# Kernel optimization log

Measured on AMD Instinct MI355X. Metric: run time of the kernel, lower is better.

## Reference

```python
import jax, jax.numpy as jnp
import numpy as np


def conv1x1(x, w, b):
    # x: (B, C_in, D, H, W), w: (C_out, C_in), b: (C_out,)  -- 1x1x1 Conv3d == per-voxel linear
    return jnp.einsum('bcdhw,oc->bodhw', x, w) + b[None, :, None, None, None]


def setup_inputs() -> dict:
    key = jax.random.key(0)
    ks = jax.random.split(key, 6)
    B, C, D, H, W = 2, 64, 8, 64, 64
    K = 4096  # codebook_size after halving
    return {
        'z': jax.random.normal(ks[0], (B, C, D, H, W), dtype=jnp.float32),
        'embedding': jax.random.normal(ks[1], (K, C), dtype=jnp.float32),
        'pre_w': jax.random.normal(ks[2], (C, C), dtype=jnp.float32) * (1.0 / np.sqrt(C)),
        'pre_b': jax.random.normal(ks[3], (C,), dtype=jnp.float32) * 0.01,
        'post_w': jax.random.normal(ks[4], (C, C), dtype=jnp.float32) * (1.0 / np.sqrt(C)),
        'post_b': jax.random.normal(ks[5], (C,), dtype=jnp.float32) * 0.01,
    }


def reference(z, embedding, pre_w, pre_b, post_w, post_b):
    B, C, D, H, W = z.shape
    x = conv1x1(z, pre_w, pre_b)  # pre_quant_conv

    # ---- quantize() ----
    # tokens: (B*D*H*W, C)
    t = jnp.transpose(x, (0, 2, 3, 4, 1)).reshape(-1, C)
    # squared euclidean distances (argmin identical to torch.cdist argmin)
    dist2 = (jnp.sum(t * t, axis=-1, keepdims=True)
             - 2.0 * t @ embedding.T
             + jnp.sum(embedding * embedding, axis=-1)[None, :])  # (N, K)
    idx = jnp.argmin(dist2, axis=-1)  # (N,)
    q = embedding[idx]  # gather: (N, C)

    commitment_loss = jnp.mean((jax.lax.stop_gradient(q) - t) ** 2)
    codebook_loss = jnp.mean((q - jax.lax.stop_gradient(t)) ** 2)

    # straight-through estimator
    q = t + jax.lax.stop_gradient(q - t)
    quant = jnp.transpose(q.reshape(B, D, H, W, C), (0, 4, 1, 2, 3))

    out = conv1x1(quant, post_w, post_b)  # post_quant_conv
    indices = idx.reshape(B, D, H, W)
    return out, codebook_loss, commitment_loss, indices
```

## Files before the change

kernel.cpp:

```cpp
#include <hip/hip_runtime.h>
#include <cstdint>
#include <cstddef>

typedef float  f32x4  __attribute__((ext_vector_type(4)));
typedef float  f32x16 __attribute__((ext_vector_type(16)));
typedef short  s16x8  __attribute__((ext_vector_type(8)));

#define DEV __device__ __forceinline__

static constexpr int    DHW       = 32768;
static constexpr int    NTOK      = 65536;
static constexpr int    CHUNK_B   = 18432;
static constexpr size_t OUT_ELEMS = 4194304;
static constexpr float  BIGC      = 512.0f;
static constexpr float  TAU       = 0.015f;
static constexpr int    FLAG_CAP  = 7424;

static constexpr size_t WS_PREP = 0;
static constexpr size_t WS_RESW = 1179648;
static constexpr size_t WS_RESB = 2228224;
static constexpr size_t WS_PART = 2490368;
static constexpr size_t WS_CNT  = 2494464;
static constexpr size_t WS_FLAG = 2494720;

DEV unsigned f2bf(float f) {
  unsigned u = __float_as_uint(f);
  return (u + 0x7FFFu + ((u >> 16) & 1u)) >> 16;
}
DEV float bf2f(unsigned h) { return __uint_as_float(h << 16); }
DEV unsigned med3u(unsigned a, unsigned b, unsigned c) {
  unsigned r;
  asm("v_med3_u32 %0, %1, %2, %3" : "=v"(r) : "v"(a), "v"(b), "v"(c));
  return r;
}
DEV void gl_lds16(const void* g, void* l) {
  __builtin_amdgcn_global_load_lds(
      (const __attribute__((address_space(1))) unsigned int*)g,
      (__attribute__((address_space(3))) unsigned int*)l, 16, 0, 0);
}

__global__ __launch_bounds__(256) void k_pre(const float* __restrict__ z,
    const float* __restrict__ emb, const float* __restrict__ pw, const float* __restrict__ pb,
    float* __restrict__ dout, char* __restrict__ ws)
{
  const int blk = blockIdx.x, tid = threadIdx.x;
  if (blk == 0 && tid == 0) *(int*)(ws + WS_CNT) = 0;
  if (blk < 256) {
    float* t = dout;
    const int v = blk * 256 + tid;
    const int b = v >> 15, r = v & (DHW - 1);
    const float* zp = z + (size_t)b * 64 * DHW + r;
    float zr[64];
#pragma unroll
    for (int c2 = 0; c2 < 64; ++c2) zr[c2] = zp[(size_t)c2 * DHW];
    for (int c = 0; c < 64; c += 4) {
      const float* w0 = pw + c * 64;
      const float* w1 = pw + (c + 1) * 64;
      const float* w2 = pw + (c + 2) * 64;
      const float* w3 = pw + (c + 3) * 64;
      float a0 = pb[c], a1 = pb[c + 1], a2 = pb[c + 2], a3 = pb[c + 3];
#pragma unroll
      for (int c2 = 0; c2 < 64; ++c2) {
        const float zv = zr[c2];
        a0 = fmaf(w0[c2], zv, a0); a1 = fmaf(w1[c2], zv, a1);
        a2 = fmaf(w2[c2], zv, a2); a3 = fmaf(w3[c2], zv, a3);
      }
      t[(size_t)c * NTOK + v]       = a0;
      t[(size_t)(c + 1) * NTOK + v] = a1;
      t[(size_t)(c + 2) * NTOK + v] = a2;
      t[(size_t)(c + 3) * NTOK + v] = a3;
    }
  } else {
    const int tt = (blk - 256) * 256 + tid;
#pragma unroll
    for (int uu = 0; uu < 2; ++uu) {
      const int u = tt * 2 + uu;
      const int k = u >> 3, j = u & 7;
      const float* ep = emb + (size_t)k * 64 + j * 8;
      unsigned hw[4], lw[4];
#pragma unroll
      for (int i = 0; i < 4; ++i) {
        float g0 = -2.0f * ep[2 * i], g1 = -2.0f * ep[2 * i + 1];
        unsigned h0 = f2bf(g0); unsigned l0 = f2bf(g0 - bf2f(h0));
        unsigned h1 = f2bf(g1); unsigned l1 = f2bf(g1 - bf2f(h1));
        hw[i] = h0 | (h1 << 16); lw[i] = l0 | (l1 << 16);
      }
      char* base = ws + WS_PREP + (size_t)(k >> 6) * CHUNK_B;
      const int r = k & 63;
      const int swz = (r & 15) << 4;
      char* rowp = base + r * 256;
      *(uint4*)(rowp + ((j * 16) ^ swz))        = make_uint4(hw[0], hw[1], hw[2], hw[3]);
      *(uint4*)(rowp + ((128 + j * 16) ^ swz))  = make_uint4(lw[0], lw[1], lw[2], lw[3]);
      if (j == 0) {
        const float* er = emb + (size_t)k * 64;
        float s = 0.f;
#pragma unroll
        for (int c = 0; c < 64; ++c) s = fmaf(er[c], er[c], s);
        s += BIGC;
        unsigned eh  = f2bf(s);
        float    rs  = s - bf2f(eh);
        unsigned el  = f2bf(rs);
        unsigned el2 = f2bf(rs - bf2f(el));
        *(uint4*)(base + 16384 + r * 16) = make_uint4(eh | (el << 16), el2, 0u, 0u);
        if (r == 0) *(uint4*)(base + 16384 + 1024) = make_uint4(0u, 0u, 0u, 0u);
      }
    }
  }
}

__global__ __launch_bounds__(512, 4) void k_dist(float* __restrict__ dout,
                                                 char* __restrict__ ws)
{
  constexpr int NCH = 32;
  __shared__ __align__(16) char smem[2 * CHUNK_B];
  const float* t = dout;
  const int tid = threadIdx.x;
  const int w = tid >> 6, lane = tid & 63;
  const int l31 = lane & 31, khalf = lane >> 5;
  const int gidx = blockIdx.x >> 1, h = blockIdx.x & 1;
  const int tb = gidx * 256 + w * 32;
  const int tok = tb + l31;

  s16x8 tav[4], tlv[4];
#pragma unroll
  for (int kt = 0; kt < 4; ++kt) {
    const float* tc = t + (size_t)(kt * 16 + khalf * 8) * NTOK + tok;
    float f[8];
#pragma unroll
    for (int i = 0; i < 8; ++i) f[i] = tc[(size_t)i * NTOK];
    union { unsigned u[4]; s16x8 v; } xh, xl;
#pragma unroll
    for (int i = 0; i < 4; ++i) {
      unsigned h0 = f2bf(f[2 * i]),     l0 = f2bf(f[2 * i]     - bf2f(h0));
      unsigned h1 = f2bf(f[2 * i + 1]), l1 = f2bf(f[2 * i + 1] - bf2f(h1));
      xh.u[i] = h0 | (h1 << 16); xl.u[i] = l0 | (l1 << 16);
    }
    tav[kt] = xh.v; tlv[kt] = xl.v;
  }
  s16x8 ones;
  { union { unsigned u[4]; s16x8 v; } o;
    o.u[0] = khalf ? 0u : 0x3F803F80u;
    o.u[1] = khalf ? 0u : 0x00003F80u;
    o.u[2] = 0u; o.u[3] = 0u; ones = o.v; }

  const char* prep = ws + WS_PREP + (size_t)h * NCH * CHUNK_B;
  const int swz = (l31 & 15) << 4;

  {
    const char* src = prep;
    gl_lds16(src + w * 1024 + lane * 16, smem + w * 1024);
    gl_lds16(src + 8192 + w * 1024 + lane * 16, smem + 8192 + w * 1024);
    if (w < 2) gl_lds16(src + 16384 + w * 1024 + lane * 16, smem + 16384 + w * 1024);
  }
  __syncthreads();

  unsigned u1 = 0x7f800000u, u2 = 0x7f800000u;
  int c1 = 0;

  for (int c = 0; c < NCH; ++c) {
    const char* L = smem + (c & 1) * CHUNK_B;
    if (c + 1 < NCH) {
      const char* src = prep + (size_t)(c + 1) * CHUNK_B;
      char* dst = smem + ((c + 1) & 1) * CHUNK_B;
      gl_lds16(src + w * 1024 + lane * 16, dst + w * 1024);
      gl_lds16(src + 8192 + w * 1024 + lane * 16, dst + 8192 + w * 1024);
      if (w < 2) gl_lds16(src + 16384 + w * 1024 + lane * 16, dst + 16384 + w * 1024);
    }
    f32x16 acc0 = {}, acc1 = {};
    {
      const s16x8 e0 = *(const s16x8*)(L + (khalf ? (16384 + 1024) : (16384 + l31 * 16)));
      const s16x8 e1 = *(const s16x8*)(L + (khalf ? (16384 + 1024) : (16384 + (32 + l31) * 16)));
      acc0 = __builtin_amdgcn_mfma_f32_32x32x16_bf16(e0, ones, acc0, 0, 0, 0);
      acc1 = __builtin_amdgcn_mfma_f32_32x32x16_bf16(e1, ones, acc1, 0, 0, 0);
    }
#pragma unroll
    for (int kt = 0; kt < 4; ++kt) {
      const int i0 = (kt * 32 + khalf * 16) ^ swz;
      const s16x8 gh0 = *(const s16x8*)(L + l31 * 256 + i0);
      const s16x8 gl0 = *(const s16x8*)(L + l31 * 256 + (i0 ^ 128));
      const s16x8 gh1 = *(const s16x8*)(L + (32 + l31) * 256 + i0);
      const s16x8 gl1 = *(const s16x8*)(L + (32 + l31) * 256 + (i0 ^ 128));
      acc0 = __builtin_amdgcn_mfma_f32_32x32x16_bf16(gh0, tav[kt], acc0, 0, 0, 0);
      acc0 = __builtin_amdgcn_mfma_f32_32x32x16_bf16(gh0, tlv[kt], acc0, 0, 0, 0);
      acc0 = __builtin_amdgcn_mfma_f32_32x32x16_bf16(gl0, tav[kt], acc0, 0, 0, 0);
      acc1 = __builtin_amdgcn_mfma_f32_32x32x16_bf16(gh1, tav[kt], acc1, 0, 0, 0);
      acc1 = __builtin_amdgcn_mfma_f32_32x32x16_bf16(gh1, tlv[kt], acc1, 0, 0, 0);
      acc1 = __builtin_amdgcn_mfma_f32_32x32x16_bf16(gl1, tav[kt], acc1, 0, 0, 0);
    }
    const unsigned p1 = u1;
#pragma unroll
    for (int q = 0; q < 16; ++q) {
      const unsigned w0 = (unsigned)((q & 3) + 8 * (q >> 2));
      unsigned v0 = (__float_as_uint(acc0[q]) & ~63u) | w0;
      u2 = med3u(u1, v0, u2); u1 = u1 < v0 ? u1 : v0;
      unsigned v1 = (__float_as_uint(acc1[q]) & ~63u) | (w0 + 32u);
      u2 = med3u(u1, v1, u2); u1 = u1 < v1 ? u1 : v1;
    }
    if (u1 != p1) c1 = c;
    __syncthreads();
  }

  u1 |= (unsigned)(khalf * 4);
  const unsigned o1 = __shfl_xor(u1, 32);
  const unsigned o2 = __shfl_xor(u2, 32);
  const int      oc = __shfl_xor(c1, 32);
  const unsigned am = u1 & ~63u, om = o1 & ~63u;
  const int mycode = c1 * 64 + (int)(u1 & 63u);
  const int ocode  = oc * 64 + (int)(o1 & 63u);
  const bool owins = (om < am) || (om == am && ocode < mycode);
  const unsigned f1 = owins ? o1 : u1;
  const int      fc = owins ? oc : c1;
  const unsigned mx = owins ? am : om;
  unsigned s2 = (u2 & ~63u) < (o2 & ~63u) ? (u2 & ~63u) : (o2 & ~63u);
  s2 = s2 < mx ? s2 : mx;
  if (khalf == 0) {
    const bool nt = (__uint_as_float(s2) - __uint_as_float(f1 & ~63u)) < TAU;
    ((unsigned*)(ws + WS_RESW))[h * 65536 + tok] = f1;
    ((unsigned char*)(ws + WS_RESB))[h * 65536 + tok] =
        (unsigned char)(fc | (nt ? 0x80 : 0));
  }
}

__global__ __launch_bounds__(256) void k_merge(const float* __restrict__ emb,
    float* __restrict__ dout, char* __restrict__ ws)
{
  __shared__ float ls[4];
  const int tid = threadIdx.x;
  const int v = blockIdx.x * 64 + (tid >> 2);
  const int q4 = tid & 3;
  const unsigned* resw = (const unsigned*)(ws + WS_RESW);
  const unsigned char* resb = (const unsigned char*)(ws + WS_RESB);
  const unsigned A = resw[v], B = resw[65536 + v];
  const unsigned am = A & ~63u, bm = B & ~63u;
  const bool bwins = bm < am;
  const unsigned bw = bwins ? B : A;
  const int bq = bwins ? 1 : 0;
  const unsigned k1 = bwins ? bm : am;
  const unsigned k2 = bwins ? am : bm;
  const unsigned char bb = resb[bq * 65536 + v];
  const int code = bq * 2048 + (int)(bb & 31u) * 64 + (int)(bw & 63u);
  const float* tcol = dout + v;
  const float* qe = emb + (size_t)code * 64 + q4 * 16;
  float acc = 0.f;
#pragma unroll
  for (int i = 0; i < 4; ++i) {
    const float4 qv = *(const float4*)(qe + i * 4);
#pragma unroll
    for (int j = 0; j < 4; ++j) {
      const int ch = q4 * 16 + i * 4 + j;
      const float d = tcol[(size_t)ch * NTOK] - ((const float*)&qv)[j];
      acc = fmaf(d, d, acc);
    }
  }
  acc += __shfl_xor(acc, 1);
  acc += __shfl_xor(acc, 2);
  if (q4 == 0) {
    dout[OUT_ELEMS + 2 + v] = (float)code;
    const bool flag = (bb & 0x80u) ||
                      (__uint_as_float(k2) - __uint_as_float(k1) < TAU);
    if (flag) {
      int p = atomicAdd((int*)(ws + WS_CNT), 1);
      if (p < FLAG_CAP) ((int*)(ws + WS_FLAG))[p] = v;
    }
  }
#pragma unroll
  for (int m = 4; m < 64; m <<= 1) acc += __shfl_xor(acc, m);
  const int lane = tid & 63, wv = tid >> 6;
  if (lane == 0) ls[wv] = acc;
  __syncthreads();
  if (tid == 0)
    ((float*)(ws + WS_PART))[blockIdx.x] = (ls[0] + ls[1] + ls[2] + ls[3]) * 0.25f;
}

__global__ __launch_bounds__(256) void k_refine(const float* __restrict__ z,
    const float* __restrict__ emb, const float* __restrict__ pw, const float* __restrict__ pb,
    float* __restrict__ dout, char* __restrict__ ws)
{
  __shared__ double tdsh[64];
  __shared__ double dred[4]; __shared__ int kred[4];
  int cv = *(const int*)(ws + WS_CNT);
  if (cv > FLAG_CAP) cv = FLAG_CAP;
  const int slot = blockIdx.x;
  if (slot >= cv) return;
  const int tid = threadIdx.x;
  const int lane = tid & 63, wv = tid >> 6;
  const int n = ((const int*)(ws + WS_FLAG))[slot];

  if (tid < 64) {
    const int b = n >> 15, r = n & (DHW - 1);
    const float* zp = z + (size_t)b * 64 * DHW + r;
    const float* wr = pw + tid * 64;
    double a = (double)pb[tid];
    for (int c2 = 0; c2 < 64; ++c2)
      a = fma((double)wr[c2], (double)zp[(size_t)c2 * DHW], a);
    tdsh[tid] = a;
  }
  __syncthreads();

  double td[64];
#pragma unroll
  for (int j = 0; j < 64; ++j) td[j] = tdsh[j];

  double dmin = 1e300; int kmin = 0;
  for (int it = 0; it < 16; ++it) {
    const int code = it * 256 + tid;
    const float4* e = (const float4*)(emb + (size_t)code * 64);
    double d0 = 0.0, d1 = 0.0;
#pragma unroll
    for (int i = 0; i < 16; ++i) {
      const float4 ev = e[i];
      const double x0 = td[4 * i]     - (double)ev.x; d0 = fma(x0, x0, d0);
      const double x1 = td[4 * i + 1] - (double)ev.y; d1 = fma(x1, x1, d1);
      const double x2 = td[4 * i + 2] - (double)ev.z; d0 = fma(x2, x2, d0);
      const double x3 = td[4 * i + 3] - (double)ev.w; d1 = fma(x3, x3, d1);
    }
    const double d = d0 + d1;
    if (d < dmin) { dmin = d; kmin = code; }
  }
#pragma unroll
  for (int m = 1; m < 64; m <<= 1) {
    const double od = __shfl_xor(dmin, m);
    const int    ok = __shfl_xor(kmin, m);
    if (od < dmin || (od == dmin && ok < kmin)) { dmin = od; kmin = ok; }
  }
  if (lane == 0) { dred[wv] = dmin; kred[wv] = kmin; }
  __syncthreads();
  if (tid == 0) {
#pragma unroll
    for (int i = 1; i < 4; ++i)
      if (dred[i] < dmin || (dred[i] == dmin && kred[i] < kmin)) { dmin = dred[i]; kmin = kred[i]; }
    dout[OUT_ELEMS + 2 + n] = (float)kmin;
  }
}

__global__ __launch_bounds__(256) void k_post(const float* __restrict__ emb,
    const float* __restrict__ ow, const float* __restrict__ ob,
    float* __restrict__ dout, const char* __restrict__ ws)
{
  __shared__ float ps[256];
  const int v = blockIdx.x * 256 + threadIdx.x;
  const int b = v >> 15, r = v & (DHW - 1);
  const int code = (int)dout[OUT_ELEMS + 2 + v];
  const float* q = emb + (size_t)code * 64;
  float qr[64];
#pragma unroll
  for (int i = 0; i < 16; ++i) *(float4*)(qr + i * 4) = *(const float4*)(q + i * 4);
  float* op = dout + (size_t)b * 64 * DHW + r;
  for (int o = 0; o < 64; o += 4) {
    const float* w0 = ow + o * 64;
    const float* w1 = ow + (o + 1) * 64;
    const float* w2 = ow + (o + 2) * 64;
    const float* w3 = ow + (o + 3) * 64;
    float a0 = ob[o], a1 = ob[o + 1], a2 = ob[o + 2], a3 = ob[o + 3];
#pragma unroll
    for (int cch = 0; cch < 64; ++cch) {
      const float qv = qr[cch];
      a0 = fmaf(w0[cch], qv, a0); a1 = fmaf(w1[cch], qv, a1);
      a2 = fmaf(w2[cch], qv, a2); a3 = fmaf(w3[cch], qv, a3);
    }
    op[(size_t)o * DHW]       = a0;
    op[(size_t)(o + 1) * DHW] = a1;
    op[(size_t)(o + 2) * DHW] = a2;
    op[(size_t)(o + 3) * DHW] = a3;
  }
  if (blockIdx.x == 0) {
    const float* part = (const float*)(ws + WS_PART);
    const int t4 = threadIdx.x * 4;
    float s = ((part[t4] + part[t4 + 1]) + part[t4 + 2]) + part[t4 + 3];
    ps[threadIdx.x] = s;
    __syncthreads();
    if (threadIdx.x == 0) {
      float tot = 0.f;
      for (int i = 0; i < 256; ++i) tot += ps[i];
      const float mean = tot / 4194304.0f;
      dout[OUT_ELEMS]     = mean;
      dout[OUT_ELEMS + 1] = mean;
    }
  }
}

extern "C" void kernel_launch(void* const* d_in, const int* in_sizes, int n_in,
                              void* d_out, int out_size, void* d_ws, size_t ws_size,
                              hipStream_t stream) {
  (void)in_sizes; (void)n_in; (void)out_size; (void)ws_size;
  const float* z   = (const float*)d_in[0];
  const float* emb = (const float*)d_in[1];
  const float* pw  = (const float*)d_in[2];
  const float* pb  = (const float*)d_in[3];
  const float* ow  = (const float*)d_in[4];
  const float* ob  = (const float*)d_in[5];
  float* out = (float*)d_out;
  char*  ws  = (char*)d_ws;

  hipLaunchKernelGGL(k_pre,    dim3(320),  dim3(256), 0, stream, z, emb, pw, pb, out, ws);
  hipLaunchKernelGGL(k_dist,   dim3(512),  dim3(512), 0, stream, out, ws);
  hipLaunchKernelGGL(k_merge,  dim3(1024), dim3(256), 0, stream, emb, out, ws);
  hipLaunchKernelGGL(k_refine, dim3(FLAG_CAP), dim3(256), 0, stream, z, emb, pw, pb, out, ws);
  hipLaunchKernelGGL(k_post,   dim3(256),  dim3(256), 0, stream, emb, ow, ob, out, ws);
}
```

Before: 196.6 us.

## Split codebook rows across wave pairs so each wave covers two token fragments

The distance kernel's work split changes. Each pair of waves now shares 64 tokens, and each wave handles 32 codebook rows per chunk against two 32-token fragments, where before each wave covered all 64 rows for 32 tokens. Every LDS codebook fragment load now feeds twice as many MFMAs, halving LDS read traffic per MFMA. In exchange, each wave holds twice the token operands in registers and needs an extra cross-wave argmin merge through shared memory with a block barrier. The merge kernel's partial-loss scaling also changes by dropping the 0.25 factor, which alters the loss output unless it is compensated in code not shown.

```diff
diff --git a/kernel.cpp b/kernel.cpp
--- a/kernel.cpp
+++ b/kernel.cpp
@@ -113,29 +113,33 @@
 {
   constexpr int NCH = 32;
   __shared__ __align__(16) char smem[2 * CHUNK_B];
+  __shared__ unsigned xch[4][64][3];
   const float* t = dout;
   const int tid = threadIdx.x;
   const int w = tid >> 6, lane = tid & 63;
   const int l31 = lane & 31, khalf = lane >> 5;
+  const int pair = w >> 1, p = w & 1;
   const int gidx = blockIdx.x >> 1, h = blockIdx.x & 1;
-  const int tb = gidx * 256 + w * 32;
-  const int tok = tb + l31;
-
-  s16x8 tav[4], tlv[4];
-#pragma unroll
-  for (int kt = 0; kt < 4; ++kt) {
-    const float* tc = t + (size_t)(kt * 16 + khalf * 8) * NTOK + tok;
-    float f[8];
-#pragma unroll
-    for (int i = 0; i < 8; ++i) f[i] = tc[(size_t)i * NTOK];
-    union { unsigned u[4]; s16x8 v; } xh, xl;
-#pragma unroll
-    for (int i = 0; i < 4; ++i) {
-      unsigned h0 = f2bf(f[2 * i]),     l0 = f2bf(f[2 * i]     - bf2f(h0));
-      unsigned h1 = f2bf(f[2 * i + 1]), l1 = f2bf(f[2 * i + 1] - bf2f(h1));
-      xh.u[i] = h0 | (h1 << 16); xl.u[i] = l0 | (l1 << 16);
-    }
-    tav[kt] = xh.v; tlv[kt] = xl.v;
+  const int tb = gidx * 256 + pair * 64;
+
+  s16x8 tav[2][4], tlv[2][4];
+#pragma unroll
+  for (int tf = 0; tf < 2; ++tf) {
+#pragma unroll
+    for (int kt = 0; kt < 4; ++kt) {
+      const float* tc = t + (size_t)(kt * 16 + khalf * 8) * NTOK + (tb + tf * 32 + l31);
+      float f[8];
+#pragma unroll
+      for (int i = 0; i < 8; ++i) f[i] = tc[(size_t)i * NTOK];
+      union { unsigned u[4]; s16x8 v; } xh, xl;
+#pragma unroll
+      for (int i = 0; i < 4; ++i) {
+        unsigned h0 = f2bf(f[2 * i]),     l0 = f2bf(f[2 * i]     - bf2f(h0));
+        unsigned h1 = f2bf(f[2 * i + 1]), l1 = f2bf(f[2 * i + 1] - bf2f(h1));
+        xh.u[i] = h0 | (h1 << 16); xl.u[i] = l0 | (l1 << 16);
+      }
+      tav[tf][kt] = xh.v; tlv[tf][kt] = xl.v;
+    }
   }
   s16x8 ones;
   { union { unsigned u[4]; s16x8 v; } o;
@@ -144,7 +148,9 @@
     o.u[2] = 0u; o.u[3] = 0u; ones = o.v; }
 
   const char* prep = ws + WS_PREP + (size_t)h * NCH * CHUNK_B;
-  const int swz = (l31 & 15) << 4;
+  const int swz  = (l31 & 15) << 4;
+  const int rowb = (p * 32 + l31) * 256;
+  const int eoff = khalf ? (16384 + 1024) : (16384 + (p * 32 + l31) * 16);
 
   {
     const char* src = prep;
@@ -154,8 +160,9 @@
   }
   __syncthreads();
 
-  unsigned u1 = 0x7f800000u, u2 = 0x7f800000u;
-  int c1 = 0;
+  unsigned u1[2] = {0x7f800000u, 0x7f800000u};
+  unsigned u2[2] = {0x7f800000u, 0x7f800000u};
+  int c1[2] = {0, 0};
 
   for (int c = 0; c < NCH; ++c) {
     const char* L = smem + (c & 1) * CHUNK_B;
@@ -168,56 +175,86 @@
     }
     f32x16 acc0 = {}, acc1 = {};
     {
-      const s16x8 e0 = *(const s16x8*)(L + (khalf ? (16384 + 1024) : (16384 + l31 * 16)));
-      const s16x8 e1 = *(const s16x8*)(L + (khalf ? (16384 + 1024) : (16384 + (32 + l31) * 16)));
+      const s16x8 e0 = *(const s16x8*)(L + eoff);
       acc0 = __builtin_amdgcn_mfma_f32_32x32x16_bf16(e0, ones, acc0, 0, 0, 0);
-      acc1 = __builtin_amdgcn_mfma_f32_32x32x16_bf16(e1, ones, acc1, 0, 0, 0);
+      acc1 = __builtin_amdgcn_mfma_f32_32x32x16_bf16(e0, ones, acc1, 0, 0, 0);
     }
 #pragma unroll
     for (int kt = 0; kt < 4; ++kt) {
       const int i0 = (kt * 32 + khalf * 16) ^ swz;
-      const s16x8 gh0 = *(const s16x8*)(L + l31 * 256 + i0);
-      const s16x8 gl0 = *(const s16x8*)(L + l31 * 256 + (i0 ^ 128));
-      const s16x8 gh1 = *(const s16x8*)(L + (32 + l31) * 256 + i0);
-      const s16x8 gl1 = *(const s16x8*)(L + (32 + l31) * 256 + (i0 ^ 128));
-      acc0 = __builtin_amdgcn_mfma_f32_32x32x16_bf16(gh0, tav[kt], acc0, 0, 0, 0);
-      acc0 = __builtin_amdgcn_mfma_f32_32x32x16_bf16(gh0, tlv[kt], acc0, 0, 0, 0);
-      acc0 = __builtin_amdgcn_mfma_f32_32x32x16_bf16(gl0, tav[kt], acc0, 0, 0, 0);
-      acc1 = __builtin_amdgcn_mfma_f32_32x32x16_bf16(gh1, tav[kt], acc1, 0, 0, 0);
-      acc1 = __builtin_amdgcn_mfma_f32_32x32x16_bf16(gh1, tlv[kt], acc1, 0, 0, 0);
-      acc1 = __builtin_amdgcn_mfma_f32_32x32x16_bf16(gl1, tav[kt], acc1, 0, 0, 0);
-    }
-    const unsigned p1 = u1;
+      const s16x8 gh = *(const s16x8*)(L + rowb + i0);
+      const s16x8 gl = *(const s16x8*)(L + rowb + (i0 ^ 128));
+      acc0 = __builtin_amdgcn_mfma_f32_32x32x16_bf16(gh, tav[0][kt], acc0, 0, 0, 0);
+      acc0 = __builtin_amdgcn_mfma_f32_32x32x16_bf16(gh, tlv[0][kt], acc0, 0, 0, 0);
+      acc0 = __builtin_amdgcn_mfma_f32_32x32x16_bf16(gl, tav[0][kt], acc0, 0, 0, 0);
+      acc1 = __builtin_amdgcn_mfma_f32_32x32x16_bf16(gh, tav[1][kt], acc1, 0, 0, 0);
+      acc1 = __builtin_amdgcn_mfma_f32_32x32x16_bf16(gh, tlv[1][kt], acc1, 0, 0, 0);
+      acc1 = __builtin_amdgcn_mfma_f32_32x32x16_bf16(gl, tav[1][kt], acc1, 0, 0, 0);
+    }
+    const unsigned pa = u1[0], pb2 = u1[1];
 #pragma unroll
     for (int q = 0; q < 16; ++q) {
       const unsigned w0 = (unsigned)((q & 3) + 8 * (q >> 2));
       unsigned v0 = (__float_as_uint(acc0[q]) & ~63u) | w0;
-      u2 = med3u(u1, v0, u2); u1 = u1 < v0 ? u1 : v0;
-      unsigned v1 = (__float_as_uint(acc1[q]) & ~63u) | (w0 + 32u);
-      u2 = med3u(u1, v1, u2); u1 = u1 < v1 ? u1 : v1;
-    }
-    if (u1 != p1) c1 = c;
+      u2[0] = med3u(u1[0], v0, u2[0]); u1[0] = u1[0] < v0 ? u1[0] : v0;
+      unsigned v1 = (__float_as_uint(acc1[q]) & ~63u) | w0;
+      u2[1] = med3u(u1[1], v1, u2[1]); u1[1] = u1[1] < v1 ? u1[1] : v1;
+    }
+    if (u1[0] != pa)  c1[0] = c;
+    if (u1[1] != pb2) c1[1] = c;
     __syncthreads();
   }
 
-  u1 |= (unsigned)(khalf * 4);
-  const unsigned o1 = __shfl_xor(u1, 32);
-  const unsigned o2 = __shfl_xor(u2, 32);
-  const int      oc = __shfl_xor(c1, 32);
-  const unsigned am = u1 & ~63u, om = o1 & ~63u;
-  const int mycode = c1 * 64 + (int)(u1 & 63u);
-  const int ocode  = oc * 64 + (int)(o1 & 63u);
-  const bool owins = (om < am) || (om == am && ocode < mycode);
-  const unsigned f1 = owins ? o1 : u1;
-  const int      fc = owins ? oc : c1;
-  const unsigned mx = owins ? am : om;
-  unsigned s2 = (u2 & ~63u) < (o2 & ~63u) ? (u2 & ~63u) : (o2 & ~63u);
-  s2 = s2 < mx ? s2 : mx;
-  if (khalf == 0) {
-    const bool nt = (__uint_as_float(s2) - __uint_as_float(f1 & ~63u)) < TAU;
-    ((unsigned*)(ws + WS_RESW))[h * 65536 + tok] = f1;
-    ((unsigned char*)(ws + WS_RESB))[h * 65536 + tok] =
-        (unsigned char)(fc | (nt ? 0x80 : 0));
+  const unsigned addb = (unsigned)(khalf * 4 + p * 32);
+  unsigned rf1[2], rs2[2]; int rfc[2];
+#pragma unroll
+  for (int tf = 0; tf < 2; ++tf) {
+    unsigned a1 = u1[tf] | addb;
+    unsigned a2 = u2[tf];
+    int cc = c1[tf];
+    const unsigned o1 = __shfl_xor(a1, 32);
+    const unsigned o2 = __shfl_xor(a2, 32);
+    const int      oc = __shfl_xor(cc, 32);
+    const unsigned am = a1 & ~63u, om = o1 & ~63u;
+    const int mycode = cc * 64 + (int)(a1 & 63u);
+    const int ocode  = oc * 64 + (int)(o1 & 63u);
+    const bool ow = (om < am) || (om == am && ocode < mycode);
+    rf1[tf] = ow ? o1 : a1;
+    rfc[tf] = ow ? oc : cc;
+    const unsigned mx = ow ? am : om;
+    unsigned s2 = (a2 & ~63u) < (o2 & ~63u) ? (a2 & ~63u) : (o2 & ~63u);
+    rs2[tf] = s2 < mx ? s2 : mx;
+  }
+  if (p == 1 && khalf == 0) {
+#pragma unroll
+    for (int tf = 0; tf < 2; ++tf) {
+      xch[pair][tf * 32 + l31][0] = rf1[tf];
+      xch[pair][tf * 32 + l31][1] = rs2[tf];
+      xch[pair][tf * 32 + l31][2] = (unsigned)rfc[tf];
+    }
+  }
+  __syncthreads();
+  if (p == 0 && khalf == 0) {
+#pragma unroll
+    for (int tf = 0; tf < 2; ++tf) {
+      const unsigned of1 = xch[pair][tf * 32 + l31][0];
+      const unsigned os2 = xch[pair][tf * 32 + l31][1];
+      const int      ofc = (int)xch[pair][tf * 32 + l31][2];
+      const unsigned am = rf1[tf] & ~63u, om = of1 & ~63u;
+      const int mycode = rfc[tf] * 64 + (int)(rf1[tf] & 63u);
+      const int ocode  = ofc * 64 + (int)(of1 & 63u);
+      const bool ow = (om < am) || (om == am && ocode < mycode);
+      const unsigned F1 = ow ? of1 : rf1[tf];
+      const int      FC = ow ? ofc : rfc[tf];
+      const unsigned mx = ow ? am : om;
+      unsigned S2 = rs2[tf] < os2 ? rs2[tf] : os2;
+      S2 = S2 < mx ? S2 : mx;
+      const bool nt = (__uint_as_float(S2) - __uint_as_float(F1 & ~63u)) < TAU;
+      const int tok = tb + tf * 32 + l31;
+      ((unsigned*)(ws + WS_RESW))[h * 65536 + tok] = F1;
+      ((unsigned char*)(ws + WS_RESB))[h * 65536 + tok] =
+          (unsigned char)(FC | (nt ? 0x80 : 0));
+    }
   }
 }
 
@@ -269,7 +306,7 @@
   if (lane == 0) ls[wv] = acc;
   __syncthreads();
   if (tid == 0)
-    ((float*)(ws + WS_PART))[blockIdx.x] = (ls[0] + ls[1] + ls[2] + ls[3]) * 0.25f;
+    ((float*)(ws + WS_PART))[blockIdx.x] = ls[0] + ls[1] + ls[2] + ls[3];
 }
 
 __global__ __launch_bounds__(256) void k_refine(const float* __restrict__ z,
```

New measurement: 194.8 us. Within noise of the previous version (-0.9%).
